# Optimization experiments

Hardware: AMD Instinct MI355X
Metric: run time of the kernel (lower is better)

Reference implementation:

```python
import jax, jax.numpy as jnp
import numpy as np

B, N, D = 2, 2048, 128
DEPTH, RECURRENCE = 3, 3
EDGE_P = 0.03  # Bernoulli edge density -> avg degree ~61


def _p(key, shape, fan_in):
    return jax.random.normal(key, shape, dtype=jnp.float32) / np.float32(np.sqrt(fan_in))


def setup_inputs() -> dict:
    key = jax.random.key(0)
    ks = jax.random.split(key, 6)
    node = jax.random.normal(ks[0], (B, N, 1), dtype=jnp.float32)
    A = (jax.random.uniform(ks[1], (B, N, N)) < EDGE_P).astype(jnp.float32)
    edge = jax.random.uniform(ks[2], (B, N, N), dtype=jnp.float32) + 0.1  # strictly positive edge weights
    inp = {"node": node, "edge": edge, "A": A}
    # (fan_in, heads) per attention layer; last layer hardcodes heads=2, concat=False
    specs = [(1, 1), (D, 1), (D, 2)]
    for l, (fin, H) in enumerate(specs):
        kk = jax.random.split(ks[3 + l], 5)
        inp[f"Wq{l}"] = _p(kk[0], (fin, H, D), fin)
        inp[f"Wk{l}"] = _p(kk[1], (fin, H, D), fin)
        inp[f"Wv{l}"] = _p(kk[2], (fin, H, D), fin)
        inp[f"We{l}"] = _p(kk[3], (H, D), 1)  # lin_edge: edge_dim=1 -> H*D, stored as (H, D)
        inp[f"Ws{l}"] = _p(kk[4], (fin, H * D if l < DEPTH - 1 else D), fin)  # root/skip lin
    return inp


def _layer_norm(x, eps=1e-5):
    mu = x.mean(-1, keepdims=True)
    var = ((x - mu) ** 2).mean(-1, keepdims=True)
    return (x - mu) / jnp.sqrt(var + eps)


def _tconv(x, e_t, mask, Wq, Wk, Wv, We, Ws, concat):
    # PyG TransformerConv (bias removed, root_weight=True):
    #   alpha_ij = softmax_j( q_i . (k_j + W_e e_ij) / sqrt(d) ) over in-neighbors j of i
    #   out_i = sum_j alpha_ij (v_j + W_e e_ij)  (+ W_skip x_i)
    # e_ij is a scalar so W_e e_ij = e_ij * We, a rank-1 term we never materialize per-edge.
    # x: (b,n,fin); e_t[b,dst,src]; We: (H,d)
    H, d = We.shape
    q = jnp.einsum('bnf,fhd->bnhd', x, Wq)
    k = jnp.einsum('bnf,fhd->bnhd', x, Wk)
    v = jnp.einsum('bnf,fhd->bnhd', x, Wv)
    scores = jnp.einsum('bihd,bjhd->bhij', q, k)  # i=dst, j=src
    qe = jnp.einsum('bihd,hd->bhi', q, We)
    scores = (scores + qe[..., None] * e_t[:, None]) / np.float32(np.sqrt(d))
    scores = jnp.where(mask[:, None], scores, jnp.finfo(scores.dtype).min)
    alpha = jax.nn.softmax(scores, axis=-1)
    alpha = jnp.where(mask[:, None], alpha, 0.0)  # isolated dst nodes aggregate to zero
    out = jnp.einsum('bhij,bjhd->bihd', alpha, v)
    ew = jnp.einsum('bhij,bij->bhi', alpha, e_t)  # sum_j alpha * e_ij
    out = out + ew.transpose(0, 2, 1)[..., None] * We
    out = out.reshape(x.shape[0], x.shape[1], H * d) if concat else out.mean(axis=2)
    return out + x @ Ws


def reference(node, edge, A, Wq0, Wk0, Wv0, We0, Ws0, Wq1, Wk1, Wv1, We1, Ws1, Wq2, Wk2, Wv2, We2, Ws2):
    e = edge * A
    e_t = jnp.swapaxes(e, 1, 2)  # e_t[b, dst, src]  (edge_index: row=src, col=dst)
    mask = e_t != 0  # dense_to_sparse keeps nonzero entries
    layers = [
        (Wq0, Wk0, Wv0, We0, Ws0, True),
        (Wq1, Wk1, Wv1, We1, Ws1, True),
        (Wq2, Wk2, Wv2, We2, Ws2, False),
    ]
    emb = node
    for r in range(RECURRENCE):
        for l in range(DEPTH):
            if r != 0 and l == 0:
                continue
            Wq, Wk, Wv, We, Ws, concat = layers[l]
            emb = _tconv(emb, e_t, mask, Wq, Wk, Wv, We, Ws, concat)
            if l != DEPTH - 1:
                emb = jax.nn.relu(_layer_norm(emb))
    return emb  # (b, n, out_dim[-1])
```

## Files before the change

### kernel.cpp

```cpp
#include <hip/hip_runtime.h>
#include <hip/hip_bf16.h>

#define BB 2
#define NN 2048
#define DD 128
#define BN (BB*NN)
#define CAP 128
#define TD 16
#define QSTR 256
#define SSTR 128
#define INV_SQRT_D 0.08838834764831845f

typedef __attribute__((ext_vector_type(8))) short short8;
typedef __attribute__((ext_vector_type(4))) float f32x4;

__device__ inline float b2f(unsigned short u) {
    union { unsigned int i; float f; } c; c.i = (unsigned int)u << 16; return c.f;
}
__device__ inline float b2f_hi(unsigned int raw) {
    union { unsigned int i; float f; } c; c.i = raw & 0xffff0000u; return c.f;
}
__device__ inline float b2f_lo(unsigned int raw) {
    union { unsigned int i; float f; } c; c.i = raw << 16; return c.f;
}

__global__ __launch_bounds__(256) void prep(
    const float* __restrict__ A, const float* __restrict__ edge,
    const float* __restrict__ node,
    const float* __restrict__ Wq0, const float* __restrict__ Wk0,
    const float* __restrict__ Wv0, const float* __restrict__ Ws0,
    const float* __restrict__ Wq1, const float* __restrict__ Wk1,
    const float* __restrict__ Wv1, const float* __restrict__ Ws1,
    const float* __restrict__ Wq2, const float* __restrict__ Wk2,
    const float* __restrict__ Wv2, const float* __restrict__ Ws2,
    __hip_bfloat16* __restrict__ Wt1, __hip_bfloat16* __restrict__ Wt2,
    float* __restrict__ q, __hip_bfloat16* __restrict__ kA,
    __hip_bfloat16* __restrict__ vA, float* __restrict__ s,
    int* __restrict__ deg, unsigned short* __restrict__ cols,
    float* __restrict__ evals)
{
    __shared__ float xnode[16];
    int bid = blockIdx.x;
    int tid = threadIdx.x;

    if (bid < BN) {
        int b   = bid >> 11;
        const size_t base = (size_t)bid * NN;
        int d0  = tid * 8;
        float4 a4 = *(const float4*)&A[base + d0];
        float4 a5 = *(const float4*)&A[base + d0 + 4];
        float4 e4 = *(const float4*)&edge[base + d0];
        float4 e5 = *(const float4*)&edge[base + d0 + 4];
        float av[8] = {a4.x, a4.y, a4.z, a4.w, a5.x, a5.y, a5.z, a5.w};
        float ew[8] = {e4.x, e4.y, e4.z, e4.w, e5.x, e5.y, e5.z, e5.w};
#pragma unroll
        for (int u = 0; u < 8; u++) {
            if (av[u] != 0.f) {
                int gdst = b * NN + d0 + u;
                int slot = atomicAdd(&deg[gdst], 1);
                if (slot < CAP) {
                    cols [(size_t)gdst * CAP + slot] = (unsigned short)bid;
                    evals[(size_t)gdst * CAP + slot] = ew[u] * av[u];
                }
            }
        }
    } else if (bid < BN + 1408) {
        int c = bid - BN;
        if (tid < DD) {
            const float *Wq, *Wk, *Wv, *Ws; __hip_bfloat16* Wt; int n, HD;
            if (c < 512) { Wq = Wq1; Wk = Wk1; Wv = Wv1; Ws = Ws1; Wt = Wt1; n = c;       HD = DD;     }
            else         { Wq = Wq2; Wk = Wk2; Wv = Wv2; Ws = Ws2; Wt = Wt2; n = c - 512; HD = 2 * DD; }
            const float* src; int ld; int col;
            if      (n < HD)     { src = Wq; col = n;          ld = HD; }
            else if (n < 2*HD)   { src = Wk; col = n - HD;     ld = HD; }
            else if (n < 3*HD)   { src = Wv; col = n - 2*HD;   ld = HD; }
            else                 { src = Ws; col = n - 3*HD;   ld = DD; }
            Wt[(size_t)n * DD + tid] = __float2bfloat16(src[(size_t)tid * ld + col]);
        }
    } else {
        int row0 = (bid - (BN + 1408)) * 16;
        if (tid < 16) xnode[tid] = node[row0 + tid];
        __syncthreads();
        for (int i = tid; i < TD * 512; i += 256) {
            int r = i >> 9, col = i & 511;
            float xv = xnode[r];
            if (col < DD) {
                q[(size_t)(row0 + r) * QSTR + col] = xv * Wq0[col];
            } else if (col < 2*DD) {
                int lc = col - DD;
                kA[(size_t)(row0 + r) * 256 + lc] = __float2bfloat16(xv * Wk0[lc]);
            } else if (col < 3*DD) {
                int lc = col - 2*DD;
                vA[(size_t)(row0 + r) * 256 + lc] = __float2bfloat16(xv * Wv0[lc]);
            } else {
                int lc = col - 3*DD;
                s[(size_t)(row0 + r) * SSTR + lc] = xv * Ws0[lc];
            }
        }
    }
}

template<int H, bool MEANH, bool LNRELU, int NCOLS, int HDN, int KVSI, int KVSO>
__global__ __launch_bounds__(1024) void fused_attn(
    float* qio,
    const __hip_bfloat16* __restrict__ k,
    const __hip_bfloat16* __restrict__ v,
    float* sio,
    const int* __restrict__ deg,
    const unsigned short* __restrict__ cols,
    const float* __restrict__ evals, const float* __restrict__ We,
    const __hip_bfloat16* __restrict__ Wt,
    __hip_bfloat16* __restrict__ kn, __hip_bfloat16* __restrict__ vn,
    float* __restrict__ out)
{
    const int HD = H * DD;
    int wid  = threadIdx.x >> 6;
    int lane = threadIdx.x & 63;
    int row0 = blockIdx.x * 16;
    int row  = row0 + wid;
    int sub  = lane >> 4;
    int s    = lane & 15;
    int c0   = lane * 2;

    __shared__ int            jc_s[16][CAP];
    __shared__ float          ev_s[16][CAP];
    __shared__ __hip_bfloat16 xs[16][136];
    int*   jc = jc_s[wid];
    float* ev = ev_s[wid];

    int dg = min(deg[row], CAP);
    for (int m = lane; m < dg; m += 64) {
        jc[m] = (int)cols[(size_t)row * CAP + m];
        ev[m] = evals[(size_t)row * CAP + m];
    }

    float qh[H][8];
    float qeI[H];
#pragma unroll
    for (int h = 0; h < H; h++) {
        const float* qp = &qio[(size_t)row * QSTR + h * DD + s * 8];
        const float* wp = &We[h * DD + s * 8];
        float pe = 0.f;
#pragma unroll
        for (int t = 0; t < 8; t++) { qh[h][t] = qp[t]; pe += qp[t] * wp[t]; }
#pragma unroll
        for (int off = 1; off < 16; off <<= 1) pe += __shfl_xor(pe, off);
        qeI[h] = pe * INV_SQRT_D;
    }

    float l_acc[H], ew_acc[H], acc[H][2];
#pragma unroll
    for (int h = 0; h < H; h++) { l_acc[h] = 0.f; ew_acc[h] = 0.f; acc[h][0] = 0.f; acc[h][1] = 0.f; }

    for (int m0 = 0; m0 < dg; m0 += 8) {
        int   e0  = m0 + sub,       e1  = m0 + 4 + sub;
        bool  ok0 = e0 < dg,        ok1 = e1 < dg;
        int   ec0 = ok0 ? e0 : m0,  ec1 = ok1 ? e1 : m0;
        int   j0  = jc[ec0],        j1  = jc[ec1];
        float ee0 = ev[ec0],        ee1 = ev[ec1];

        int jb[8];
#pragma unroll
        for (int es = 0; es < 8; es++) jb[es] = jc[(m0 + es < dg) ? m0 + es : m0];

        unsigned int vraw[H][8];
#pragma unroll
        for (int h = 0; h < H; h++)
#pragma unroll
            for (int es = 0; es < 8; es++)
                vraw[h][es] = *(const unsigned int*)&v[(size_t)jb[es] * KVSI + h * DD + c0];
        short8 kk0[H], kk1[H];
#pragma unroll
        for (int h = 0; h < H; h++) {
            kk0[h] = *(const short8*)&k[(size_t)j0 * KVSI + h * DD + s * 8];
            kk1[h] = *(const short8*)&k[(size_t)j1 * KVSI + h * DD + s * 8];
        }

#pragma unroll
        for (int h = 0; h < H; h++) {
            float p0 = qh[h][0]*b2f((unsigned short)kk0[h][0]) + qh[h][1]*b2f((unsigned short)kk0[h][1])
                     + qh[h][2]*b2f((unsigned short)kk0[h][2]) + qh[h][3]*b2f((unsigned short)kk0[h][3])
                     + qh[h][4]*b2f((unsigned short)kk0[h][4]) + qh[h][5]*b2f((unsigned short)kk0[h][5])
                     + qh[h][6]*b2f((unsigned short)kk0[h][6]) + qh[h][7]*b2f((unsigned short)kk0[h][7]);
            float p1 = qh[h][0]*b2f((unsigned short)kk1[h][0]) + qh[h][1]*b2f((unsigned short)kk1[h][1])
                     + qh[h][2]*b2f((unsigned short)kk1[h][2]) + qh[h][3]*b2f((unsigned short)kk1[h][3])
                     + qh[h][4]*b2f((unsigned short)kk1[h][4]) + qh[h][5]*b2f((unsigned short)kk1[h][5])
                     + qh[h][6]*b2f((unsigned short)kk1[h][6]) + qh[h][7]*b2f((unsigned short)kk1[h][7]);
#pragma unroll
            for (int off = 1; off < 16; off <<= 1) {
                p0 += __shfl_xor(p0, off);
                p1 += __shfl_xor(p1, off);
            }
            float sc0 = ok0 ? (p0 * INV_SQRT_D + qeI[h] * ee0) : -1e30f;
            float sc1 = ok1 ? (p1 * INV_SQRT_D + qeI[h] * ee1) : -1e30f;
            float a0 = __expf(fminf(sc0, 60.f));
            float a1 = __expf(fminf(sc1, 60.f));
            l_acc[h]  += a0 + a1;
            ew_acc[h] += a0 * ee0 + a1 * ee1;
            float al0[4], al1[4];
#pragma unroll
            for (int es = 0; es < 4; es++) { al0[es] = __shfl(a0, es * 16); al1[es] = __shfl(a1, es * 16); }
#pragma unroll
            for (int es = 0; es < 4; es++) {
                acc[h][0] += al0[es] * b2f_lo(vraw[h][es]) + al1[es] * b2f_lo(vraw[h][es + 4]);
                acc[h][1] += al0[es] * b2f_hi(vraw[h][es]) + al1[es] * b2f_hi(vraw[h][es + 4]);
            }
        }
    }

    float rh[H][2];
#pragma unroll
    for (int h = 0; h < H; h++) {
        float l  = l_acc[h]  + __shfl_xor(l_acc[h], 16);
        float ew = ew_acc[h] + __shfl_xor(ew_acc[h], 16);
        l  += __shfl_xor(l, 32);
        ew += __shfl_xor(ew, 32);
        float invZ = (l > 0.f) ? 1.f / l : 0.f;
        rh[h][0] = (acc[h][0] + ew * We[h * DD + c0])     * invZ;
        rh[h][1] = (acc[h][1] + ew * We[h * DD + c0 + 1]) * invZ;
    }
    float r0, r1;
    if constexpr (MEANH) {
        r0 = 0.5f * (rh[0][0] + rh[H - 1][0]);
        r1 = 0.5f * (rh[0][1] + rh[H - 1][1]);
    } else {
        r0 = rh[0][0]; r1 = rh[0][1];
    }
    float2 sk = *(const float2*)&sio[(size_t)row * SSTR + c0];
    r0 += sk.x; r1 += sk.y;

    if constexpr (LNRELU) {
        float sum = r0 + r1, sq = r0 * r0 + r1 * r1;
#pragma unroll
        for (int off = 32; off; off >>= 1) { sum += __shfl_xor(sum, off); sq += __shfl_xor(sq, off); }
        float mu  = sum * (1.f / DD);
        float var = sq * (1.f / DD) - mu * mu;
        float rs  = rsqrtf(var + 1e-5f);
        r0 = fmaxf((r0 - mu) * rs, 0.f);
        r1 = fmaxf((r1 - mu) * rs, 0.f);
    }

    if constexpr (NCOLS == 0) {
        float2 res; res.x = r0; res.y = r1;
        *(float2*)&out[(size_t)row * DD + c0] = res;
    } else {
        __hip_bfloat162 o;
        o.x = __float2bfloat16(r0);
        o.y = __float2bfloat16(r1);
        *(__hip_bfloat162*)&xs[wid][c0] = o;
        __syncthreads();

        int m16 = lane & 15, quad = lane >> 4;
        short8 a[4];
#pragma unroll
        for (int ks = 0; ks < 4; ks++)
            a[ks] = *(const short8*)&xs[m16][ks * 32 + quad * 8];

#pragma unroll 1
        for (int tile = wid; tile < NCOLS / 16; tile += 16) {
            int n0 = tile * 16;
            f32x4 pacc = {0.f, 0.f, 0.f, 0.f};
#pragma unroll
            for (int ks = 0; ks < 4; ks++) {
                const short8* bp = (const short8*)&Wt[(size_t)(n0 + m16) * DD + ks * 32 + quad * 8];
                pacc = __builtin_amdgcn_mfma_f32_16x16x32_bf16(a[ks], *bp, pacc, 0, 0, 0);
            }
            if (n0 < HDN) {
#pragma unroll
                for (int r = 0; r < 4; r++)
                    qio[(size_t)(row0 + quad * 4 + r) * QSTR + n0 + m16] = pacc[r];
            } else if (n0 < 2*HDN) {
                int lc = n0 - HDN;
#pragma unroll
                for (int r = 0; r < 4; r++)
                    kn[(size_t)(row0 + quad * 4 + r) * KVSO + lc + m16] = __float2bfloat16(pacc[r]);
            } else if (n0 < 3*HDN) {
                int lc = n0 - 2*HDN;
#pragma unroll
                for (int r = 0; r < 4; r++)
                    vn[(size_t)(row0 + quad * 4 + r) * KVSO + lc + m16] = __float2bfloat16(pacc[r]);
            } else {
                int lc = n0 - 3*HDN;
#pragma unroll
                for (int r = 0; r < 4; r++)
                    sio[(size_t)(row0 + quad * 4 + r) * SSTR + lc + m16] = pacc[r];
            }
        }
    }
}

extern "C" void kernel_launch(void* const* d_in, const int* in_sizes, int n_in,
                              void* d_out, int out_size, void* d_ws, size_t ws_size,
                              hipStream_t stream)
{
    const float* node = (const float*)d_in[0];
    const float* edge = (const float*)d_in[1];
    const float* A    = (const float*)d_in[2];
    const float* Wq[3] = {(const float*)d_in[3],  (const float*)d_in[8],  (const float*)d_in[13]};
    const float* Wk[3] = {(const float*)d_in[4],  (const float*)d_in[9],  (const float*)d_in[14]};
    const float* Wv[3] = {(const float*)d_in[5],  (const float*)d_in[10], (const float*)d_in[15]};
    const float* We[3] = {(const float*)d_in[6],  (const float*)d_in[11], (const float*)d_in[16]};
    const float* Ws[3] = {(const float*)d_in[7],  (const float*)d_in[12], (const float*)d_in[17]};

    char* p = (char*)d_ws;
    float*          q  = (float*)p;          p += (size_t)BN * QSTR * 4;
    float*          s  = (float*)p;          p += (size_t)BN * SSTR * 4;
    __hip_bfloat16* kA = (__hip_bfloat16*)p; p += (size_t)BN * 256 * 2;
    __hip_bfloat16* vA = (__hip_bfloat16*)p; p += (size_t)BN * 256 * 2;
    __hip_bfloat16* kB = (__hip_bfloat16*)p; p += (size_t)BN * 128 * 2;
    __hip_bfloat16* vB = (__hip_bfloat16*)p; p += (size_t)BN * 128 * 2;
    __hip_bfloat16* Wt1 = (__hip_bfloat16*)p; p += (size_t)512 * DD * 2;
    __hip_bfloat16* Wt2 = (__hip_bfloat16*)p; p += (size_t)896 * DD * 2;
    int*            degb = (int*)p;            p += (size_t)BN * 4;
    float*          evb  = (float*)p;          p += (size_t)BN * CAP * 4;
    unsigned short* colb = (unsigned short*)p; p += (size_t)BN * CAP * 2;

    hipMemsetAsync(degb, 0, (size_t)BN * 4, stream);
    prep<<<BN + 1408 + BN / 16, 256, 0, stream>>>(
        A, edge, node,
        Wq[0], Wk[0], Wv[0], Ws[0],
        Wq[1], Wk[1], Wv[1], Ws[1],
        Wq[2], Wk[2], Wv[2], Ws[2],
        Wt1, Wt2, q, kA, vA, s, degb, colb, evb);

    fused_attn<1, false, true, 512, 128, 256, 128><<<BN / 16, 1024, 0, stream>>>(
        q, kA, vA, s, degb, colb, evb, We[0], Wt1, kB, vB, nullptr);
    fused_attn<1, false, true, 896, 256, 128, 256><<<BN / 16, 1024, 0, stream>>>(
        q, kB, vB, s, degb, colb, evb, We[1], Wt2, kA, vA, nullptr);
    fused_attn<2, true, false, 512, 128, 256, 128><<<BN / 16, 1024, 0, stream>>>(
        q, kA, vA, s, degb, colb, evb, We[2], Wt1, kB, vB, nullptr);
    fused_attn<1, false, true, 896, 256, 128, 256><<<BN / 16, 1024, 0, stream>>>(
        q, kB, vB, s, degb, colb, evb, We[1], Wt2, kA, vA, nullptr);
    fused_attn<2, true, false, 512, 128, 256, 128><<<BN / 16, 1024, 0, stream>>>(
        q, kA, vA, s, degb, colb, evb, We[2], Wt1, kB, vB, nullptr);
    fused_attn<1, false, true, 896, 256, 128, 256><<<BN / 16, 1024, 0, stream>>>(
        q, kB, vB, s, degb, colb, evb, We[1], Wt2, kA, vA, nullptr);
    fused_attn<2, true, false, 0, 0, 256, 0><<<BN / 16, 1024, 0, stream>>>(
        q, kA, vA, s, degb, colb, evb, We[2], nullptr, nullptr, nullptr, (float*)d_out);
}
```

Baseline: 338.8 us.

## Build per-destination adjacency lists in shared memory, dropping global atomics and memset

```diff
diff --git a/kernel.cpp b/kernel.cpp
--- a/kernel.cpp
+++ b/kernel.cpp
@@ -39,33 +39,55 @@
     int* __restrict__ deg, unsigned short* __restrict__ cols,
     float* __restrict__ evals)
 {
+    __shared__ int   cnt[TD];
+    __shared__ int   csh[TD][CAP];
+    __shared__ float esh[TD][CAP];
     __shared__ float xnode[16];
+
     int bid = blockIdx.x;
     int tid = threadIdx.x;
 
-    if (bid < BN) {
-        int b   = bid >> 11;
-        const size_t base = (size_t)bid * NN;
-        int d0  = tid * 8;
-        float4 a4 = *(const float4*)&A[base + d0];
-        float4 a5 = *(const float4*)&A[base + d0 + 4];
-        float4 e4 = *(const float4*)&edge[base + d0];
-        float4 e5 = *(const float4*)&edge[base + d0 + 4];
-        float av[8] = {a4.x, a4.y, a4.z, a4.w, a5.x, a5.y, a5.z, a5.w};
-        float ew[8] = {e4.x, e4.y, e4.z, e4.w, e5.x, e5.y, e5.z, e5.w};
-#pragma unroll
-        for (int u = 0; u < 8; u++) {
-            if (av[u] != 0.f) {
-                int gdst = b * NN + d0 + u;
-                int slot = atomicAdd(&deg[gdst], 1);
-                if (slot < CAP) {
-                    cols [(size_t)gdst * CAP + slot] = (unsigned short)bid;
-                    evals[(size_t)gdst * CAP + slot] = ew[u] * av[u];
+    if (bid < 256) {
+        int b    = bid >> 7;
+        int dst0 = (bid & 127) * TD;
+
+        if (tid < TD) cnt[tid] = 0;
+        __syncthreads();
+
+        int srcOff = tid >> 2;
+        int dOff   = (tid & 3) * 4;
+        const size_t base = (size_t)b * NN * NN + dst0 + dOff;
+
+#pragma unroll 2
+        for (int s0 = 0; s0 < NN; s0 += 64) {
+            int src = s0 + srcOff;
+            float4 a4 = *(const float4*)&A[base + (size_t)src * NN];
+            float4 e4 = *(const float4*)&edge[base + (size_t)src * NN];
+            int gsrc = b * NN + src;
+            float av[4] = {a4.x, a4.y, a4.z, a4.w};
+            float ev[4] = {e4.x, e4.y, e4.z, e4.w};
+#pragma unroll
+            for (int u = 0; u < 4; u++) {
+                if (av[u] != 0.f) {
+                    int d = dOff + u;
+                    int slot = atomicAdd(&cnt[d], 1);
+                    if (slot < CAP) { csh[d][slot] = gsrc; esh[d][slot] = ev[u] * av[u]; }
                 }
             }
         }
-    } else if (bid < BN + 1408) {
-        int c = bid - BN;
+        __syncthreads();
+
+        if (tid < TD) deg[b * NN + dst0 + tid] = min(cnt[tid], CAP);
+        for (int idx = tid; idx < TD * CAP; idx += 256) {
+            int d = idx / CAP, i = idx % CAP;
+            if (i < min(cnt[d], CAP)) {
+                size_t row = (size_t)(b * NN + dst0 + d);
+                cols [row * CAP + i] = (unsigned short)csh[d][i];
+                evals[row * CAP + i] = esh[d][i];
+            }
+        }
+    } else if (bid < 256 + 1408) {
+        int c = bid - 256;
         if (tid < DD) {
             const float *Wq, *Wk, *Wv, *Ws; __hip_bfloat16* Wt; int n, HD;
             if (c < 512) { Wq = Wq1; Wk = Wk1; Wv = Wv1; Ws = Ws1; Wt = Wt1; n = c;       HD = DD;     }
@@ -78,7 +100,7 @@
             Wt[(size_t)n * DD + tid] = __float2bfloat16(src[(size_t)tid * ld + col]);
         }
     } else {
-        int row0 = (bid - (BN + 1408)) * 16;
+        int row0 = (bid - (256 + 1408)) * 16;
         if (tid < 16) xnode[tid] = node[row0 + tid];
         __syncthreads();
         for (int i = tid; i < TD * 512; i += 256) {
@@ -315,8 +337,7 @@
     float*          evb  = (float*)p;          p += (size_t)BN * CAP * 4;
     unsigned short* colb = (unsigned short*)p; p += (size_t)BN * CAP * 2;
 
-    hipMemsetAsync(degb, 0, (size_t)BN * 4, stream);
-    prep<<<BN + 1408 + BN / 16, 256, 0, stream>>>(
+    prep<<<256 + 1408 + BN / 16, 256, 0, stream>>>(
         A, edge, node,
         Wq[0], Wk[0], Wv[0], Ws[0],
         Wq[1], Wk[1], Wv[1], Ws[1],
```

Measured after the change: 320.9 us. 1.06x faster.
